# Performance work log

Hardware: AMD Instinct MI355X
Metric: run time of the kernel (lower is better)

Reference implementation:

```python
import jax, jax.numpy as jnp
import numpy as np

EPS = 1e-5

def setup_inputs() -> dict:
    key = jax.random.key(0)
    ks = jax.random.split(key, 7)
    C = 512
    x = jax.random.normal(ks[0], (16, C, 32, 32), dtype=jnp.float32)
    gn_w = jax.random.normal(ks[1], (C,), dtype=jnp.float32) * 0.02 + 1.0
    gn_b = jax.random.normal(ks[2], (C,), dtype=jnp.float32) * 0.02
    qkv_w = jax.random.normal(ks[3], (3 * C, C), dtype=jnp.float32) * (1.0 / np.sqrt(C))
    qkv_b = jax.random.normal(ks[4], (3 * C,), dtype=jnp.float32) * 0.02
    proj_w = jax.random.normal(ks[5], (C, C), dtype=jnp.float32) * (1.0 / np.sqrt(C))
    proj_b = jax.random.normal(ks[6], (C,), dtype=jnp.float32) * 0.02
    return {"x": x, "gn_w": gn_w, "gn_b": gn_b, "qkv_w": qkv_w,
            "qkv_b": qkv_b, "proj_w": proj_w, "proj_b": proj_b}

def reference(x, gn_w, gn_b, qkv_w, qkv_b, proj_w, proj_b):
    B, C, H, W = x.shape
    S = H * W
    # GroupNorm with 1 group: normalize over (C,H,W) per sample
    mean = jnp.mean(x, axis=(1, 2, 3), keepdims=True)
    var = jnp.var(x, axis=(1, 2, 3), keepdims=True)
    h = (x - mean) * jax.lax.rsqrt(var + EPS)
    h = h * gn_w[None, :, None, None] + gn_b[None, :, None, None]
    # 1x1 conv qkv: [B,C,H,W] -> [B,3C,H,W], flatten spatial -> [B,S,3C]
    hf = h.reshape(B, C, S)  # b c s
    qkv = jnp.einsum('bcs,oc->bso', hf, qkv_w) + qkv_b  # [B,S,3C]
    q, k, v = jnp.split(qkv, 3, axis=-1)  # each [B,S,C]
    scale = C ** (-0.5)
    attn = jax.nn.softmax(jnp.einsum('bqc,bkc->bqk', q, k) * scale, axis=-1)
    out = jnp.einsum('bqk,bkc->bqc', attn, v)  # [B,S,C]
    out = jnp.einsum('bsc,oc->bso', out, proj_w) + proj_b
    out = out.transpose(0, 2, 1).reshape(B, C, H, W)
    return x + out
```

## Files before the change

kernel.cpp:

```cpp
#include <hip/hip_runtime.h>
#include <stdint.h>

#define B_  16
#define C_  512
#define S_  1024
#define NSAMP (C_*S_)

typedef __bf16 bf16x8 __attribute__((ext_vector_type(8)));
typedef float  f32x4  __attribute__((ext_vector_type(4)));

__device__ __forceinline__ float bf2f(uint16_t u){ return __uint_as_float(((uint32_t)u)<<16); }
__device__ __forceinline__ uint16_t f2bf(float f){
  uint32_t u = __float_as_uint(f);
  uint32_t r = u + 0x7fffu + ((u>>16)&1u);
  return (uint16_t)(r>>16);
}
__device__ __forceinline__ float wsum(float v){
  #pragma unroll
  for(int o=32;o;o>>=1) v += __shfl_xor(v,o,64);
  return v;
}
__device__ __forceinline__ int wsumi(int v){
  #pragma unroll
  for(int o=32;o;o>>=1) v += __shfl_xor(v,o,64);
  return v;
}
__device__ __forceinline__ void gload16(const void* g, void* l){
  __builtin_amdgcn_global_load_lds(
      (__attribute__((address_space(1))) void*)g,
      (__attribute__((address_space(3))) void*)l, 16, 0, 0);
}

__device__ __forceinline__ void convseg(const void* src, uint16_t* dst, int n, int f, int t){
  const int idx = t*8;
  if (idx >= n) return;
  if (f){
    const float* s = (const float*)src;
    float4 v0 = *(const float4*)(s + idx);
    float4 v1 = *(const float4*)(s + idx + 4);
    ushort4 a, b;
    a.x=f2bf(v0.x); a.y=f2bf(v0.y); a.z=f2bf(v0.z); a.w=f2bf(v0.w);
    b.x=f2bf(v1.x); b.y=f2bf(v1.y); b.z=f2bf(v1.z); b.w=f2bf(v1.w);
    *(ushort4*)(dst + idx)     = a;
    *(ushort4*)(dst + idx + 4) = b;
  } else {
    *(uint4*)(dst + idx) = *(const uint4*)((const uint16_t*)src + idx);
  }
}
__global__ __launch_bounds__(256) void prep_k(
    const void* __restrict__ srcx, uint16_t* __restrict__ xb, float2* __restrict__ part,
    const void* qkvw, const void* projw, const void* gnw, const void* gnb,
    const void* qkvb, const void* projb,
    uint16_t* qkvwb, uint16_t* projwb, uint16_t* gnwb, uint16_t* gnbb,
    uint16_t* qkvbb, uint16_t* projbb, int* __restrict__ flag){
  const int t = threadIdx.x;
  __shared__ int sdet[4];
  int f;
  {
    const uint4 v = ((const uint4*)srcx)[t & 255];
    uint32_t ww[4] = {v.x, v.y, v.z, v.w};
    int c = 0;
    #pragma unroll
    for(int q=0;q<4;q++) c += ((((ww[q] & 0xffffu) >> 7) & 0xffu) >= 132) ? 1 : 0;
    c = wsumi(c);
    if ((t & 63) == 0) sdet[t >> 6] = c;
    __syncthreads();
    f = (sdet[0] + sdet[1] + sdet[2] + sdet[3] > 128) ? 1 : 0;
  }
  if (blockIdx.x == 0 && t == 0) *flag = f;

  if (blockIdx.x >= 1024){
    const int bid = blockIdx.x - 1024;
    if (bid < 384){
      const size_t off = (size_t)bid*2048;
      convseg((const char*)qkvw + off*(f?4:2), qkvwb + off, 2048, f, t);
    } else if (bid < 512){
      const size_t off = (size_t)(bid-384)*2048;
      convseg((const char*)projw + off*(f?4:2), projwb + off, 2048, f, t);
    } else {
      convseg(gnw,   gnwb,   512,  f, t);
      convseg(gnb,   gnbb,   512,  f, t);
      convseg(qkvb,  qkvbb,  1536, f, t);
      convseg(projb, projbb, 512,  f, t);
    }
    return;
  }
  const size_t base = (size_t)blockIdx.x * 8192;
  float s = 0.f, s2 = 0.f;
  if (f){
    const float4* sp = (const float4*)((const float*)srcx + base);
    ushort4* dp = (ushort4*)(xb + base);
    #pragma unroll
    for(int i=0;i<8;i++){
      float4 v = sp[i*256 + t];
      s  += v.x + v.y + v.z + v.w;
      s2 += v.x*v.x + v.y*v.y + v.z*v.z + v.w*v.w;
      ushort4 o; o.x=f2bf(v.x); o.y=f2bf(v.y); o.z=f2bf(v.z); o.w=f2bf(v.w);
      dp[i*256 + t] = o;
    }
  } else {
    const uint4* sp = (const uint4*)((const uint16_t*)srcx + base);
    uint4* dp = (uint4*)(xb + base);
    #pragma unroll
    for(int i=0;i<4;i++){
      uint4 p = sp[i*256 + t];
      dp[i*256 + t] = p;
      uint32_t uu[4] = {p.x,p.y,p.z,p.w};
      #pragma unroll
      for(int q=0;q<4;q++){
        float f0 = __uint_as_float(uu[q]<<16);
        float f1 = __uint_as_float(uu[q] & 0xffff0000u);
        s += f0 + f1; s2 += f0*f0 + f1*f1;
      }
    }
  }
  s = wsum(s); s2 = wsum(s2);
  __shared__ float rs[4], rq[4];
  const int lane = t & 63, w = t >> 6;
  if (lane==0){ rs[w]=s; rq[w]=s2; }
  __syncthreads();
  if (t==0)
    part[blockIdx.x] = make_float2(rs[0]+rs[1]+rs[2]+rs[3], rq[0]+rq[1]+rq[2]+rq[3]);
}

__global__ __launch_bounds__(256) void gn_apply_t(const uint16_t* __restrict__ x,
    const uint16_t* __restrict__ gw, const uint16_t* __restrict__ gb,
    const float2* __restrict__ part, uint16_t* __restrict__ hT){
  __shared__ float tile[64*129];
  const int b = blockIdx.z, c0 = blockIdx.y<<6, s0 = blockIdx.x<<7;
  const int t = threadIdx.x;
  float2 p = part[b*64 + (t & 63)];
  float s = wsum(p.x), s2 = wsum(p.y);
  const float ninv = 1.f/(float)NSAMP;
  const float mn = s*ninv;
  const float rstd = rsqrtf(s2*ninv - mn*mn + 1e-5f);
  #pragma unroll
  for(int k=0;k<4;k++){
    const int ci = t + k*256;
    const int cl = ci>>4, sc = ci&15;
    uint4 v = *(const uint4*)&x[((size_t)b*C_ + c0+cl)*S_ + s0 + sc*8];
    const uint16_t* e = (const uint16_t*)&v;
    float* dst = &tile[cl*129 + sc*8];
    #pragma unroll
    for(int q=0;q<8;q++) dst[q] = bf2f(e[q]);
  }
  __syncthreads();
  const int cc = t & 7;
  const int sb0 = t >> 3;
  uint4 wv4 = *(const uint4*)&gw[c0 + cc*8];
  uint4 bv4 = *(const uint4*)&gb[c0 + cc*8];
  const uint16_t* we = (const uint16_t*)&wv4;
  const uint16_t* be = (const uint16_t*)&bv4;
  float aq[8], cq[8];
  #pragma unroll
  for(int q=0;q<8;q++){ aq[q] = bf2f(we[q])*rstd; cq[q] = bf2f(be[q]) - mn*aq[q]; }
  #pragma unroll
  for(int k=0;k<4;k++){
    const int sl = sb0 + k*32;
    uint16_t ov[8];
    #pragma unroll
    for(int q=0;q<8;q++){
      float xv = tile[(cc*8+q)*129 + sl];
      ov[q] = f2bf(xv*aq[q] + cq[q]);
    }
    uint4 o;
    o.x = (uint32_t)ov[0] | ((uint32_t)ov[1]<<16);
    o.y = (uint32_t)ov[2] | ((uint32_t)ov[3]<<16);
    o.z = (uint32_t)ov[4] | ((uint32_t)ov[5]<<16);
    o.w = (uint32_t)ov[6] | ((uint32_t)ov[7]<<16);
    *(uint4*)&hT[((size_t)b*S_ + s0+sl)*C_ + c0 + cc*8] = o;
  }
}

__global__ __launch_bounds__(256)
void qkv_k(const uint16_t* __restrict__ hT, const uint16_t* __restrict__ qkvw,
           const uint16_t* __restrict__ qkvb, uint16_t* __restrict__ qk,
           uint16_t* __restrict__ Vt)
{
  __shared__ uint16_t smem[32768];
  const int tid = threadIdx.x;
  const int lane = tid & 63, w = tid >> 6;
  const int quad = lane >> 4, lm = lane & 15;
  const int wm = (w & 1) << 6, wn = (w >> 1) << 6;

  const bool vpath = blockIdx.x >= 1024;
  const int id = vpath ? (blockIdx.x - 1024) : blockIdx.x;
  const int r8 = id & 7, k8 = id >> 3;
  int m0, n0, bz;
  const uint16_t *Abase, *Bbase;
  if (!vpath){
    const int g = r8*16 + (k8 & 15);
    m0 = g << 7; n0 = (k8 >> 4) << 7; bz = 0;
    Abase = hT + (size_t)m0*512;
    Bbase = qkvw + (size_t)n0*512;
  } else {
    const int g = r8*16 + (k8 & 15);
    m0 = (k8 >> 4) << 7; n0 = (g & 7) << 7; bz = g >> 3;
    Abase = qkvw + (size_t)(1024 + m0)*512;
    Bbase = hT + (size_t)bz*S_*C_ + (size_t)n0*512;
  }

  f32x4 acc[4][4];
  #pragma unroll
  for(int i=0;i<4;i++)
    #pragma unroll
    for(int j=0;j<4;j++) acc[i][j] = (f32x4){0.f,0.f,0.f,0.f};

  const int srow = tid >> 3;
  const int sx   = (tid & 7) ^ (srow & 7);
  const uint16_t* ga = Abase + (size_t)srow*512 + sx*8;
  const uint16_t* gb = Bbase + (size_t)srow*512 + sx*8;
  uint16_t* sa0 = &smem[tid*8];
  uint16_t* sb0 = &smem[8192 + tid*8];
  uint16_t* sa1 = &smem[16384 + tid*8];
  uint16_t* sb1 = &smem[24576 + tid*8];

  #pragma unroll
  for(int i=0;i<4;i++){
    gload16(ga + (size_t)(i*32)*512, sa0 + i*2048);
    gload16(gb + (size_t)(i*32)*512, sb0 + i*2048);
  }
  for(int t=0;t<8;t++){
    if (t < 7){
      uint16_t* na = (t&1) ? sa0 : sa1;
      uint16_t* nb = (t&1) ? sb0 : sb1;
      const int k1 = (t+1)<<6;
      #pragma unroll
      for(int i=0;i<4;i++){
        gload16(ga + (size_t)(i*32)*512 + k1, na + i*2048);
        gload16(gb + (size_t)(i*32)*512 + k1, nb + i*2048);
      }
      asm volatile("s_waitcnt vmcnt(8)" ::: "memory");
    } else {
      asm volatile("s_waitcnt vmcnt(0)" ::: "memory");
    }
    __builtin_amdgcn_s_barrier();
    __builtin_amdgcn_sched_barrier(0);
    const int boff = (t&1) << 14;
    #pragma unroll
    for(int kk=0;kk<64;kk+=32){
      bf16x8 av[4], bv[4];
      #pragma unroll
      for(int i=0;i<4;i++){
        const int row = wm + i*16 + lm;
        av[i] = *(const bf16x8*)&smem[boff + row*64 + ((((kk>>3)+quad) ^ (row&7))<<3)];
      }
      #pragma unroll
      for(int j=0;j<4;j++){
        const int row = wn + j*16 + lm;
        bv[j] = *(const bf16x8*)&smem[boff + 8192 + row*64 + ((((kk>>3)+quad) ^ (row&7))<<3)];
      }
      #pragma unroll
      for(int i=0;i<4;i++)
        #pragma unroll
        for(int j=0;j<4;j++)
          acc[i][j] = __builtin_amdgcn_mfma_f32_16x16x32_bf16(av[i], bv[j], acc[i][j], 0,0,0);
    }
    __builtin_amdgcn_s_barrier();
  }

  uint16_t* Cs = smem;
  if (!vpath){
    #pragma unroll
    for(int j=0;j<4;j++){
      const int col_l = wn + j*16 + lm;
      const float bvv = bf2f(qkvb[n0 + col_l]);
      #pragma unroll
      for(int i=0;i<4;i++){
        const int rl0 = wm + i*16 + (quad<<2);
        #pragma unroll
        for(int r=0;r<4;r++)
          Cs[(rl0+r)*128 + col_l] = f2bf(acc[i][j][r] + bvv);
      }
    }
  } else {
    #pragma unroll
    for(int i=0;i<4;i++){
      const int rl0 = wm + i*16 + (quad<<2);
      #pragma unroll
      for(int r=0;r<4;r++){
        const float bvv = bf2f(qkvb[1024 + m0 + rl0 + r]);
        #pragma unroll
        for(int j=0;j<4;j++)
          Cs[(rl0+r)*128 + wn + j*16 + lm] = f2bf(acc[i][j][r] + bvv);
      }
    }
  }
  __syncthreads();
  uint16_t* base = vpath ? (Vt + (size_t)bz*C_*S_) : qk;
  #pragma unroll
  for(int k=0;k<8;k++){
    const int ci = tid + k*256;
    const int rl = ci>>4, ccc = ci&15;
    *(uint4*)&base[(size_t)(m0+rl)*1024 + n0 + ccc*8] = *(const uint4*)&Cs[rl*128 + ccc*8];
  }
}

__global__ __launch_bounds__(512)
void fa_k(const uint16_t* __restrict__ qk, const uint16_t* __restrict__ Vt,
          uint16_t* __restrict__ out)
{
  extern __shared__ char smem[];
  uint16_t* Qs = (uint16_t*)smem;
  char* Pb = smem + 65536;
  char* ST = smem + 81920;
  float* RS = (float*)(smem + 147456);

  const int tid = threadIdx.x;
  const int w = tid >> 6, lane = tid & 63;
  const int quad = lane >> 4, lm = lane & 15;
  const int wq = w & 1, wk = w >> 1;

  const int wg = (blockIdx.x & 7)*32 + (blockIdx.x >> 3);
  const int bz = wg >> 4;
  const int q0 = (wg & 15) << 6;

  const uint16_t* qbase = qk + ((size_t)bz*1024 + q0)*1024;
  const uint16_t* kbase = qk + (size_t)bz*1024*1024 + 512;
  const uint16_t* vbase = Vt + ((size_t)bz*512 + w*64)*1024;

  f32x4 o[4][4];
  #pragma unroll
  for(int i=0;i<4;i++)
    #pragma unroll
    for(int j=0;j<4;j++) o[i][j] = (f32x4){0.f,0.f,0.f,0.f};
  float rsacc[2][4];
  #pragma unroll
  for(int i=0;i<2;i++)
    #pragma unroll
    for(int r=0;r<4;r++) rsacc[i][r] = 0.f;

  auto stage_k = [&](int kt, int ch){
    #pragma unroll
    for (int g=0; g<2; ++g){
      const int idx = g*512 + tid;
      const int row = idx >> 3, c8 = idx & 7;
      gload16(kbase + (size_t)(kt*128 + row)*1024 + ch*64 + ((c8 ^ (row&7))<<3),
              ST + ((ch&3)<<14) + idx*16);
    }
  };
  auto stage_v = [&](int kt, int kk){
    #pragma unroll
    for (int g=0; g<4; ++g){
      const int idx = g*64 + lane;
      const int c = idx >> 2, c4 = idx & 3;
      gload16(vbase + (size_t)c*1024 + kt*128 + kk*32 + ((c4 ^ (c&3))<<3),
              ST + ((kk&1)<<15) + (w<<12) + idx*16);
    }
  };

  #pragma unroll
  for (int rd=0; rd<8; ++rd){
    const int row = rd*8 + (tid>>6), chunk = tid & 63;
    const int scol = (chunk & 56) | ((chunk & 7) ^ (row & 7));
    gload16(qbase + (size_t)row*1024 + scol*8, (char*)Qs + rd*8192 + tid*16);
  }
  stage_k(0,0); stage_k(0,1); stage_k(0,2);

  for (int kt=0; kt<8; ++kt){
    f32x4 s[2][2];
    #pragma unroll
    for(int i=0;i<2;i++)
      #pragma unroll
      for(int j=0;j<2;j++) s[i][j] = (f32x4){0.f,0.f,0.f,0.f};

    #pragma unroll
    for (int ch=0; ch<8; ++ch){
      if (ch==6) asm volatile("s_waitcnt vmcnt(2)" ::: "memory");
      else       asm volatile("s_waitcnt vmcnt(4)" ::: "memory");
      __builtin_amdgcn_s_barrier();
      __builtin_amdgcn_sched_barrier(0);
      if (ch < 5) stage_k(kt, ch+3);
      if (ch == 6) stage_v(kt, 0);
      const int slot = (ch&3)<<14;
      #pragma unroll
      for (int kk=0; kk<2; ++kk){
        bf16x8 av[2], bv[2];
        #pragma unroll
        for (int i=0;i<2;i++){
          const int q = wq*32 + i*16 + lm;
          av[i] = *(const bf16x8*)((const char*)Qs + q*1024 + (ch*8 + (((kk<<2)+quad) ^ (q&7)))*16);
        }
        #pragma unroll
        for (int j=0;j<2;j++){
          const int key = wk*32 + j*16 + lm;
          bv[j] = *(const bf16x8*)(ST + slot + key*128 + ((((kk<<2)+quad) ^ (key&7))<<4));
        }
        #pragma unroll
        for (int i=0;i<2;i++)
          #pragma unroll
          for (int j=0;j<2;j++)
            s[i][j] = __builtin_amdgcn_mfma_f32_16x16x32_bf16(av[i], bv[j], s[i][j], 0,0,0);
      }
    }

    #pragma unroll
    for (int i=0;i<2;i++)
      #pragma unroll
      for (int j=0;j<2;j++)
        #pragma unroll
        for (int r=0;r<4;r++){
          const int q = wq*32 + i*16 + (quad<<2) + r;
          const int col = wk*32 + j*16 + lm;
          const float pv = __expf(s[i][j][r] * 0.044194173824159216f);
          rsacc[i][r] += pv;
          const int cch = col >> 3;
          const int chs = (cch & 8) | ((cch & 7) ^ (q & 7));
          *(uint16_t*)(Pb + q*256 + chs*16 + ((col & 7)<<1)) = f2bf(pv);
        }
    asm volatile("s_waitcnt lgkmcnt(0)" ::: "memory");
    __builtin_amdgcn_sched_barrier(0);
    __builtin_amdgcn_s_barrier();
    __builtin_amdgcn_sched_barrier(0);
    stage_v(kt, 1);

    #pragma unroll
    for (int kk=0; kk<4; ++kk){
      if (kk<3) asm volatile("s_waitcnt vmcnt(4)" ::: "memory");
      else      asm volatile("s_waitcnt vmcnt(0)" ::: "memory");
      __builtin_amdgcn_sched_barrier(0);
      bf16x8 pa[4], bv[4];
      #pragma unroll
      for (int i=0;i<4;i++){
        const int q = i*16 + lm;
        const int cch = (kk<<2) + quad;
        const int chs = (cch & 8) | ((cch & 7) ^ (q & 7));
        pa[i] = *(const bf16x8*)(Pb + q*256 + chs*16);
      }
      #pragma unroll
      for (int j=0;j<4;j++){
        const int c = j*16 + lm;
        bv[j] = *(const bf16x8*)(ST + ((kk&1)<<15) + (w<<12) + c*64 + ((quad ^ (c&3))<<4));
      }
      #pragma unroll
      for (int i=0;i<4;i++)
        #pragma unroll
        for (int j=0;j<4;j++)
          o[i][j] = __builtin_amdgcn_mfma_f32_16x16x32_bf16(pa[i], bv[j], o[i][j], 0,0,0);
      __builtin_amdgcn_sched_barrier(0);
      if (kk<2) stage_v(kt, kk+2);
    }
    __builtin_amdgcn_s_barrier();
    if (kt < 7){ stage_k(kt+1,0); stage_k(kt+1,1); stage_k(kt+1,2); }
  }

  #pragma unroll
  for (int i=0;i<2;i++)
    #pragma unroll
    for (int r=0;r<4;r++){
      float v = rsacc[i][r];
      #pragma unroll
      for (int off=1; off<16; off<<=1) v += __shfl_xor(v, off, 64);
      rsacc[i][r] = v;
    }
  if (lm == 0){
    #pragma unroll
    for (int i=0;i<2;i++)
      #pragma unroll
      for (int r=0;r<4;r++){
        const int q = wq*32 + i*16 + (quad<<2) + r;
        RS[q*4 + wk] = rsacc[i][r];
      }
  }
  asm volatile("s_waitcnt lgkmcnt(0)" ::: "memory");
  __builtin_amdgcn_sched_barrier(0);
  __builtin_amdgcn_s_barrier();
  __builtin_amdgcn_sched_barrier(0);
  float inv_[4][4];
  #pragma unroll
  for (int i=0;i<4;i++)
    #pragma unroll
    for (int r=0;r<4;r++){
      const int q = i*16 + (quad<<2) + r;
      f32x4 rv = *(const f32x4*)&RS[q*4];
      inv_[i][r] = 1.f / (rv[0]+rv[1]+rv[2]+rv[3]);
    }
  uint16_t* Cs = Qs;
  #pragma unroll
  for (int i=0;i<4;i++)
    #pragma unroll
    for (int j=0;j<4;j++)
      #pragma unroll
      for (int r=0;r<4;r++){
        const int row = i*16 + (quad<<2) + r;
        const int col = (w<<6) + j*16 + lm;
        Cs[row*512 + col] = f2bf(o[i][j][r] * inv_[i][r]);
      }
  __syncthreads();
  #pragma unroll
  for (int rd=0; rd<8; ++rd){
    const int idx = rd*512 + tid;
    const int row = idx >> 6, cc = idx & 63;
    *(uint4*)&out[((size_t)bz*1024 + q0 + row)*512 + cc*8] =
        *(const uint4*)((const char*)Cs + row*1024 + cc*16);
  }
}

template<bool HASBIAS, bool BIASROW, bool OUTDYN, bool HASRES, int SWZMODE, bool EXP>
__global__ __launch_bounds__(256)
void gemm_bt(const uint16_t* __restrict__ A, const uint16_t* __restrict__ Bt,
             void* __restrict__ Cp, const uint16_t* __restrict__ bias,
             const uint16_t* __restrict__ xres, const int* __restrict__ flag,
             int lda, int ldb, int ldc, int K,
             long long sA, long long sB, long long sC)
{
  __shared__ uint16_t smem[32768];
  const int lin = (blockIdx.z * gridDim.y + blockIdx.y) * gridDim.x + blockIdx.x;
  const int r8 = lin & 7, kk8 = lin >> 3;
  int bx, by, bz;
  if (SWZMODE == 0){
    const int G = (gridDim.y * gridDim.z) >> 3;
    const int g = r8 * G + (kk8 % G);
    bx = kk8 / G; by = g % gridDim.y; bz = g / gridDim.y;
  } else {
    const int G = (gridDim.x * gridDim.z) >> 3;
    const int g = r8 * G + (kk8 % G);
    by = kk8 / G; bx = g % gridDim.x; bz = g / gridDim.x;
  }

  const int tid = threadIdx.x;
  const int lane = tid & 63, w = tid >> 6;
  const int quad = lane >> 4, lm = lane & 15;
  const int m0 = by << 7, n0 = bx << 7;
  A  += (size_t)bz * sA;
  Bt += (size_t)bz * sB;

  f32x4 acc[4][4];
  #pragma unroll
  for(int i=0;i<4;i++)
    #pragma unroll
    for(int j=0;j<4;j++) acc[i][j] = (f32x4){0.f,0.f,0.f,0.f};

  const int wm = (w & 1) << 6, wn = (w >> 1) << 6;
  const int srow = tid >> 3;
  const int sx   = (tid & 7) ^ (srow & 7);
  const uint16_t* ga = A  + (size_t)(m0 + srow)*lda + sx*8;
  const uint16_t* gb = Bt + (size_t)(n0 + srow)*ldb + sx*8;
  uint16_t* sa0 = &smem[tid*8];
  uint16_t* sb0 = &smem[8192 + tid*8];
  uint16_t* sa1 = &smem[16384 + tid*8];
  uint16_t* sb1 = &smem[24576 + tid*8];

  const int NT = K >> 6;
  #pragma unroll
  for(int i=0;i<4;i++){
    gload16(ga + (size_t)(i*32)*lda, sa0 + i*2048);
    gload16(gb + (size_t)(i*32)*ldb, sb0 + i*2048);
  }
  for(int t=0;t<NT;t++){
    if (t < NT-1){
      uint16_t* na = (t&1) ? sa0 : sa1;
      uint16_t* nb = (t&1) ? sb0 : sb1;
      const int k1 = (t+1)<<6;
      #pragma unroll
      for(int i=0;i<4;i++){
        gload16(ga + (size_t)(i*32)*lda + k1, na + i*2048);
        gload16(gb + (size_t)(i*32)*ldb + k1, nb + i*2048);
      }
      asm volatile("s_waitcnt vmcnt(8)" ::: "memory");
    } else {
      asm volatile("s_waitcnt vmcnt(0)" ::: "memory");
    }
    __builtin_amdgcn_s_barrier();
    __builtin_amdgcn_sched_barrier(0);
    const int boff = (t&1) << 14;
    #pragma unroll
    for(int kk=0;kk<64;kk+=32){
      bf16x8 av[4], bv[4];
      #pragma unroll
      for(int i=0;i<4;i++){
        const int row = wm + i*16 + lm;
        av[i] = *(const bf16x8*)&smem[boff + row*64 + ((((kk>>3)+quad) ^ (row&7))<<3)];
      }
      #pragma unroll
      for(int j=0;j<4;j++){
        const int row = wn + j*16 + lm;
        bv[j] = *(const bf16x8*)&smem[boff + 8192 + row*64 + ((((kk>>3)+quad) ^ (row&7))<<3)];
      }
      #pragma unroll
      for(int i=0;i<4;i++)
        #pragma unroll
        for(int j=0;j<4;j++)
          acc[i][j] = __builtin_amdgcn_mfma_f32_16x16x32_bf16(av[i], bv[j], acc[i][j], 0,0,0);
    }
    __builtin_amdgcn_s_barrier();
  }

  const size_t cb = (size_t)bz * (size_t)sC;
  if (!OUTDYN && !HASRES){
    uint16_t* Cs = smem;
    #pragma unroll
    for(int j=0;j<4;j++){
      const int col_l = wn + j*16 + lm;
      const float cbias = (HASBIAS && !BIASROW) ? bf2f(bias[n0 + col_l]) : 0.f;
      #pragma unroll
      for(int i=0;i<4;i++){
        const int rl0 = wm + i*16 + (quad<<2);
        #pragma unroll
        for(int r=0;r<4;r++){
          float v = acc[i][j][r] + cbias;
          if (HASBIAS && BIASROW) v += bf2f(bias[m0 + rl0 + r]);
          if (EXP) v = __expf(v * 0.044194173824159216f);
          Cs[(rl0+r)*128 + col_l] = f2bf(v);
        }
      }
    }
    __syncthreads();
    uint16_t* base = (uint16_t*)Cp + cb;
    #pragma unroll
    for(int k=0;k<8;k++){
      const int ci = tid + k*256;
      const int rl = ci>>4, cc = ci&15;
      *(uint4*)&base[(size_t)(m0+rl)*ldc + n0 + cc*8] = *(const uint4*)&Cs[rl*128 + cc*8];
    }
  } else {
    float* Cs32 = (float*)smem;
    const int f = OUTDYN ? *flag : 0;
    const int wnh = wn >> 1;
    #pragma unroll
    for(int half=0; half<2; ++half){
      #pragma unroll
      for(int j2=0;j2<2;j2++){
        const int j = half*2 + j2;
        const int col_l = wn + j*16 + lm;
        const int hcol = wnh + j2*16 + lm;
        const float cbias = (HASBIAS && !BIASROW) ? bf2f(bias[n0 + col_l]) : 0.f;
        #pragma unroll
        for(int i=0;i<4;i++){
          const int rl0 = wm + i*16 + (quad<<2);
          #pragma unroll
          for(int r=0;r<4;r++){
            float v = acc[i][j][r] + cbias;
            if (HASBIAS && BIASROW) v += bf2f(bias[m0 + rl0 + r]);
            if (EXP) v = __expf(v * 0.044194173824159216f);
            Cs32[(rl0+r)*64 + hcol] = v;
          }
        }
      }
      __syncthreads();
      #pragma unroll
      for(int k=0;k<8;k++){
        const int ci = tid + k*256;
        const int rl = ci>>4, c4 = ci&15;
        float4 vv = *(const float4*)&Cs32[rl*64 + c4*4];
        const int gcol = n0 + c4*4 + ((c4>=8)?32:0) + half*32;
        const size_t idx = cb + (size_t)(m0+rl)*ldc + gcol;
        float o0=vv.x, o1=vv.y, o2=vv.z, o3=vv.w;
        if (HASRES){
          uint2 rr = *(const uint2*)&xres[idx];
          o0 += bf2f((uint16_t)(rr.x & 0xffffu));
          o1 += bf2f((uint16_t)(rr.x >> 16));
          o2 += bf2f((uint16_t)(rr.y & 0xffffu));
          o3 += bf2f((uint16_t)(rr.y >> 16));
        }
        if (OUTDYN && f){
          float4 oo = make_float4(o0,o1,o2,o3);
          *(float4*)&((float*)Cp)[idx] = oo;
        } else {
          uint2 oo;
          oo.x = (uint32_t)f2bf(o0) | ((uint32_t)f2bf(o1)<<16);
          oo.y = (uint32_t)f2bf(o2) | ((uint32_t)f2bf(o3)<<16);
          *(uint2*)&((uint16_t*)Cp)[idx] = oo;
        }
      }
      __syncthreads();
    }
  }
}

extern "C" void kernel_launch(void* const* d_in, const int* in_sizes, int n_in,
                              void* d_out, int out_size, void* d_ws, size_t ws_size,
                              hipStream_t stream){
  char* ws = (char*)d_ws;
  int*      flag  = (int*)ws;
  float2*   part  = (float2*)(ws + 4096);
  uint16_t* gnwb  = (uint16_t*)(ws + 16384);
  uint16_t* gnbb  = (uint16_t*)(ws + 17408);
  uint16_t* qkvbb = (uint16_t*)(ws + 18432);
  uint16_t* projbb= (uint16_t*)(ws + 21504);
  uint16_t* qkvwb = (uint16_t*)(ws + 32768);
  uint16_t* projwb= (uint16_t*)(ws + 1605632);
  uint16_t* xb    = (uint16_t*)(ws + 4194304);
  uint16_t* hT    = (uint16_t*)(ws + 20971520);
  uint16_t* qk    = (uint16_t*)(ws + 37748736);
  uint16_t* Vt    = (uint16_t*)(ws + 104857600);

  static bool attr_done = false;
  if (!attr_done){
    (void)hipFuncSetAttribute(reinterpret_cast<const void*>(fa_k),
                              hipFuncAttributeMaxDynamicSharedMemorySize, 148480);
    attr_done = true;
  }

  hipLaunchKernelGGL(prep_k, dim3(1537), dim3(256), 0, stream,
                     d_in[0], xb, part,
                     d_in[3], d_in[5], d_in[1], d_in[2], d_in[4], d_in[6],
                     qkvwb, projwb, gnwb, gnbb, qkvbb, projbb, flag);
  hipLaunchKernelGGL(gn_apply_t, dim3(8,8,16), dim3(256), 0, stream, xb, gnwb, gnbb, part, hT);

  hipLaunchKernelGGL(qkv_k, dim3(1536), dim3(256), 0, stream, hT, qkvwb, qkvbb, qk, Vt);

  hipLaunchKernelGGL(fa_k, dim3(256), dim3(512), 148480, stream, qk, Vt, hT);

  hipLaunchKernelGGL((gemm_bt<true,true,true,true,1,false>), dim3(8,4,16), dim3(256), 0, stream,
      projwb, hT, d_out, projbb, xb, flag,
      512, 512, 1024, 512, 0LL, (long long)S_*C_, (long long)C_*S_);
}
```

Measured before the change: 205.2 us.

## Warp-specialize attention kernel into QK^T and PV wavefront groups

The attention kernel grows from 512 to 1024 threads and splits its wavefronts into two groups. Eight wavefronts compute QK^T and softmax numerators into a double-buffered P tile, while the other eight run the PV MFMAs one key tile behind, so the two phases overlap instead of being separated by block-wide barriers. Q is now read straight from global memory into registers rather than staged in LDS, and each wavefront stages its own K or V slices in private LDS buffers. The trade-offs are higher register pressure under launch_bounds(1024), a larger LDS footprint, and repeated global reads of Q.

```diff
diff --git a/kernel.cpp b/kernel.cpp
--- a/kernel.cpp
+++ b/kernel.cpp
@@ -296,28 +296,35 @@
   }
 }
 
-__global__ __launch_bounds__(512)
+__global__ __launch_bounds__(1024, 4)
 void fa_k(const uint16_t* __restrict__ qk, const uint16_t* __restrict__ Vt,
           uint16_t* __restrict__ out)
 {
   extern __shared__ char smem[];
-  uint16_t* Qs = (uint16_t*)smem;
-  char* Pb = smem + 65536;
-  char* ST = smem + 81920;
-  float* RS = (float*)(smem + 147456);
+  char* KST = smem;
+  char* VST = smem + 65536;
+  char* Pb  = smem + 131072;
+  float* RS = (float*)Pb;
 
   const int tid = threadIdx.x;
   const int w = tid >> 6, lane = tid & 63;
   const int quad = lane >> 4, lm = lane & 15;
-  const int wq = w & 1, wk = w >> 1;
 
   const int wg = (blockIdx.x & 7)*32 + (blockIdx.x >> 3);
   const int bz = wg >> 4;
   const int q0 = (wg & 15) << 6;
 
-  const uint16_t* qbase = qk + ((size_t)bz*1024 + q0)*1024;
+  const bool isQKT = (w < 8);
+  const int wq = w & 1, wk = (w >> 1) & 3;
+  const int pw = w & 7;
+
   const uint16_t* kbase = qk + (size_t)bz*1024*1024 + 512;
-  const uint16_t* vbase = Vt + ((size_t)bz*512 + w*64)*1024;
+  const uint16_t* qrow0 = qk + ((size_t)bz*1024 + q0 + wq*32 + lm)*1024 + quad*8;
+  const uint16_t* qrow1 = qrow0 + (size_t)16*1024;
+  const uint16_t* vbase = Vt + ((size_t)bz*512 + pw*64)*1024;
+
+  char* kpriv = KST + w*8192;
+  char* vpriv = VST + pw*8192;
 
   f32x4 o[4][4];
   #pragma unroll
@@ -330,166 +337,163 @@
     #pragma unroll
     for(int r=0;r<4;r++) rsacc[i][r] = 0.f;
 
-  auto stage_k = [&](int kt, int ch){
-    #pragma unroll
-    for (int g=0; g<2; ++g){
-      const int idx = g*512 + tid;
+  auto stage_kp = [&](int kt, int ch){
+    char* dst = kpriv + ((ch&1)<<12);
+    #pragma unroll
+    for (int g=0; g<4; ++g){
+      const int idx = g*64 + lane;
       const int row = idx >> 3, c8 = idx & 7;
-      gload16(kbase + (size_t)(kt*128 + row)*1024 + ch*64 + ((c8 ^ (row&7))<<3),
-              ST + ((ch&3)<<14) + idx*16);
+      gload16(kbase + (size_t)(kt*128 + wk*32 + row)*1024 + ch*64 + ((c8 ^ (row&7))<<3),
+              dst + idx*16);
     }
   };
-  auto stage_v = [&](int kt, int kk){
+  auto stage_vp = [&](int kt, int kk){
+    char* dst = vpriv + ((kk&1)<<12);
     #pragma unroll
     for (int g=0; g<4; ++g){
       const int idx = g*64 + lane;
       const int c = idx >> 2, c4 = idx & 3;
       gload16(vbase + (size_t)c*1024 + kt*128 + kk*32 + ((c4 ^ (c&3))<<3),
-              ST + ((kk&1)<<15) + (w<<12) + idx*16);
+              dst + idx*16);
     }
   };
 
-  #pragma unroll
-  for (int rd=0; rd<8; ++rd){
-    const int row = rd*8 + (tid>>6), chunk = tid & 63;
-    const int scol = (chunk & 56) | ((chunk & 7) ^ (row & 7));
-    gload16(qbase + (size_t)row*1024 + scol*8, (char*)Qs + rd*8192 + tid*16);
-  }
-  stage_k(0,0); stage_k(0,1); stage_k(0,2);
-
-  for (int kt=0; kt<8; ++kt){
-    f32x4 s[2][2];
-    #pragma unroll
-    for(int i=0;i<2;i++)
-      #pragma unroll
-      for(int j=0;j<2;j++) s[i][j] = (f32x4){0.f,0.f,0.f,0.f};
-
-    #pragma unroll
-    for (int ch=0; ch<8; ++ch){
-      if (ch==6) asm volatile("s_waitcnt vmcnt(2)" ::: "memory");
-      else       asm volatile("s_waitcnt vmcnt(4)" ::: "memory");
-      __builtin_amdgcn_s_barrier();
-      __builtin_amdgcn_sched_barrier(0);
-      if (ch < 5) stage_k(kt, ch+3);
-      if (ch == 6) stage_v(kt, 0);
-      const int slot = (ch&3)<<14;
-      #pragma unroll
-      for (int kk=0; kk<2; ++kk){
-        bf16x8 av[2], bv[2];
-        #pragma unroll
-        for (int i=0;i<2;i++){
-          const int q = wq*32 + i*16 + lm;
-          av[i] = *(const bf16x8*)((const char*)Qs + q*1024 + (ch*8 + (((kk<<2)+quad) ^ (q&7)))*16);
+  if (isQKT) stage_kp(0, 0);
+
+  for (int t=0; t<9; ++t){
+    __builtin_amdgcn_s_barrier();
+    if (isQKT){
+      if (t < 8){
+        f32x4 s[2][2];
+        #pragma unroll
+        for(int i=0;i<2;i++)
+          #pragma unroll
+          for(int j=0;j<2;j++) s[i][j] = (f32x4){0.f,0.f,0.f,0.f};
+        char* Pw = Pb + ((t&1)<<14);
+        #pragma unroll
+        for (int ch=0; ch<8; ++ch){
+          if (ch < 7)      stage_kp(t, ch+1);
+          else if (t < 7)  stage_kp(t+1, 0);
+          asm volatile("s_waitcnt vmcnt(4)" ::: "memory");
+          __builtin_amdgcn_sched_barrier(0);
+          const bf16x8 a00 = *(const bf16x8*)(qrow0 + ch*64);
+          const bf16x8 a10 = *(const bf16x8*)(qrow1 + ch*64);
+          const bf16x8 a01 = *(const bf16x8*)(qrow0 + ch*64 + 32);
+          const bf16x8 a11 = *(const bf16x8*)(qrow1 + ch*64 + 32);
+          const char* kslot = kpriv + ((ch&1)<<12);
+          #pragma unroll
+          for (int kk=0; kk<2; ++kk){
+            const int sw = (((kk<<2)+quad) ^ (lm&7)) << 4;
+            bf16x8 bv0 = *(const bf16x8*)(kslot + lm*128 + sw);
+            bf16x8 bv1 = *(const bf16x8*)(kslot + (16+lm)*128 + sw);
+            const bf16x8 A0 = kk ? a01 : a00;
+            const bf16x8 A1 = kk ? a11 : a10;
+            s[0][0] = __builtin_amdgcn_mfma_f32_16x16x32_bf16(A0, bv0, s[0][0], 0,0,0);
+            s[0][1] = __builtin_amdgcn_mfma_f32_16x16x32_bf16(A0, bv1, s[0][1], 0,0,0);
+            s[1][0] = __builtin_amdgcn_mfma_f32_16x16x32_bf16(A1, bv0, s[1][0], 0,0,0);
+            s[1][1] = __builtin_amdgcn_mfma_f32_16x16x32_bf16(A1, bv1, s[1][1], 0,0,0);
+          }
         }
         #pragma unroll
-        for (int j=0;j<2;j++){
-          const int key = wk*32 + j*16 + lm;
-          bv[j] = *(const bf16x8*)(ST + slot + key*128 + ((((kk<<2)+quad) ^ (key&7))<<4));
+        for (int i=0;i<2;i++)
+          #pragma unroll
+          for (int j=0;j<2;j++)
+            #pragma unroll
+            for (int r=0;r<4;r++){
+              const int q = wq*32 + i*16 + (quad<<2) + r;
+              const int col = wk*32 + j*16 + lm;
+              const float pv = __expf(s[i][j][r] * 0.044194173824159216f);
+              rsacc[i][r] += pv;
+              const int cch = col >> 3;
+              const int chs = (cch & 8) | ((cch & 7) ^ (q & 7));
+              *(uint16_t*)(Pw + q*256 + chs*16 + ((col & 7)<<1)) = f2bf(pv);
+            }
+        asm volatile("s_waitcnt lgkmcnt(0)" ::: "memory");
+      } else {
+        #pragma unroll
+        for (int i=0;i<2;i++)
+          #pragma unroll
+          for (int r=0;r<4;r++){
+            float v = rsacc[i][r];
+            #pragma unroll
+            for (int off=1; off<16; off<<=1) v += __shfl_xor(v, off, 64);
+            rsacc[i][r] = v;
+          }
+        if (lm == 0){
+          #pragma unroll
+          for (int i=0;i<2;i++)
+            #pragma unroll
+            for (int r=0;r<4;r++){
+              const int q = wq*32 + i*16 + (quad<<2) + r;
+              RS[q*4 + wk] = rsacc[i][r];
+            }
         }
-        #pragma unroll
-        for (int i=0;i<2;i++)
-          #pragma unroll
-          for (int j=0;j<2;j++)
-            s[i][j] = __builtin_amdgcn_mfma_f32_16x16x32_bf16(av[i], bv[j], s[i][j], 0,0,0);
-      }
-    }
-
-    #pragma unroll
-    for (int i=0;i<2;i++)
-      #pragma unroll
-      for (int j=0;j<2;j++)
+        asm volatile("s_waitcnt lgkmcnt(0)" ::: "memory");
+      }
+    } else {
+      if (t > 0){
+        const int kt = t-1;
+        const char* Pr = Pb + ((kt&1)<<14);
+        stage_vp(kt, 0);
+        stage_vp(kt, 1);
+        #pragma unroll
+        for (int kk=0; kk<4; ++kk){
+          if (kk < 3) asm volatile("s_waitcnt vmcnt(4)" ::: "memory");
+          else        asm volatile("s_waitcnt vmcnt(0)" ::: "memory");
+          __builtin_amdgcn_sched_barrier(0);
+          bf16x8 pa[4], bv[4];
+          #pragma unroll
+          for (int i=0;i<4;i++){
+            const int q = i*16 + lm;
+            const int cch = (kk<<2) + quad;
+            const int chs = (cch & 8) | ((cch & 7) ^ (q & 7));
+            pa[i] = *(const bf16x8*)(Pr + q*256 + chs*16);
+          }
+          #pragma unroll
+          for (int j=0;j<4;j++){
+            const int c = j*16 + lm;
+            bv[j] = *(const bf16x8*)(vpriv + ((kk&1)<<12) + c*64 + ((quad ^ (c&3))<<4));
+          }
+          #pragma unroll
+          for (int i=0;i<4;i++)
+            #pragma unroll
+            for (int j=0;j<4;j++)
+              o[i][j] = __builtin_amdgcn_mfma_f32_16x16x32_bf16(pa[i], bv[j], o[i][j], 0,0,0);
+          __builtin_amdgcn_sched_barrier(0);
+          if (kk < 2) stage_vp(kt, kk+2);
+        }
+      }
+    }
+  }
+
+  __builtin_amdgcn_s_barrier();
+  uint16_t* Cs = (uint16_t*)smem;
+  if (!isQKT){
+    float inv_[4][4];
+    #pragma unroll
+    for (int i=0;i<4;i++)
+      #pragma unroll
+      for (int r=0;r<4;r++){
+        const int q = i*16 + (quad<<2) + r;
+        f32x4 rv = *(const f32x4*)&RS[q*4];
+        inv_[i][r] = 1.f / (rv[0]+rv[1]+rv[2]+rv[3]);
+      }
+    #pragma unroll
+    for (int i=0;i<4;i++)
+      #pragma unroll
+      for (int j=0;j<4;j++)
         #pragma unroll
         for (int r=0;r<4;r++){
-          const int q = wq*32 + i*16 + (quad<<2) + r;
-          const int col = wk*32 + j*16 + lm;
-          const float pv = __expf(s[i][j][r] * 0.044194173824159216f);
-          rsacc[i][r] += pv;
-          const int cch = col >> 3;
-          const int chs = (cch & 8) | ((cch & 7) ^ (q & 7));
-          *(uint16_t*)(Pb + q*256 + chs*16 + ((col & 7)<<1)) = f2bf(pv);
+          const int row = i*16 + (quad<<2) + r;
+          const int col = pw*64 + j*16 + lm;
+          Cs[row*512 + col] = f2bf(o[i][j][r] * inv_[i][r]);
         }
-    asm volatile("s_waitcnt lgkmcnt(0)" ::: "memory");
-    __builtin_amdgcn_sched_barrier(0);
-    __builtin_amdgcn_s_barrier();
-    __builtin_amdgcn_sched_barrier(0);
-    stage_v(kt, 1);
-
-    #pragma unroll
-    for (int kk=0; kk<4; ++kk){
-      if (kk<3) asm volatile("s_waitcnt vmcnt(4)" ::: "memory");
-      else      asm volatile("s_waitcnt vmcnt(0)" ::: "memory");
-      __builtin_amdgcn_sched_barrier(0);
-      bf16x8 pa[4], bv[4];
-      #pragma unroll
-      for (int i=0;i<4;i++){
-        const int q = i*16 + lm;
-        const int cch = (kk<<2) + quad;
-        const int chs = (cch & 8) | ((cch & 7) ^ (q & 7));
-        pa[i] = *(const bf16x8*)(Pb + q*256 + chs*16);
-      }
-      #pragma unroll
-      for (int j=0;j<4;j++){
-        const int c = j*16 + lm;
-        bv[j] = *(const bf16x8*)(ST + ((kk&1)<<15) + (w<<12) + c*64 + ((quad ^ (c&3))<<4));
-      }
-      #pragma unroll
-      for (int i=0;i<4;i++)
-        #pragma unroll
-        for (int j=0;j<4;j++)
-          o[i][j] = __builtin_amdgcn_mfma_f32_16x16x32_bf16(pa[i], bv[j], o[i][j], 0,0,0);
-      __builtin_amdgcn_sched_barrier(0);
-      if (kk<2) stage_v(kt, kk+2);
-    }
-    __builtin_amdgcn_s_barrier();
-    if (kt < 7){ stage_k(kt+1,0); stage_k(kt+1,1); stage_k(kt+1,2); }
-  }
-
-  #pragma unroll
-  for (int i=0;i<2;i++)
-    #pragma unroll
-    for (int r=0;r<4;r++){
-      float v = rsacc[i][r];
-      #pragma unroll
-      for (int off=1; off<16; off<<=1) v += __shfl_xor(v, off, 64);
-      rsacc[i][r] = v;
-    }
-  if (lm == 0){
-    #pragma unroll
-    for (int i=0;i<2;i++)
-      #pragma unroll
-      for (int r=0;r<4;r++){
-        const int q = wq*32 + i*16 + (quad<<2) + r;
-        RS[q*4 + wk] = rsacc[i][r];
-      }
   }
   asm volatile("s_waitcnt lgkmcnt(0)" ::: "memory");
-  __builtin_amdgcn_sched_barrier(0);
   __builtin_amdgcn_s_barrier();
-  __builtin_amdgcn_sched_barrier(0);
-  float inv_[4][4];
-  #pragma unroll
-  for (int i=0;i<4;i++)
-    #pragma unroll
-    for (int r=0;r<4;r++){
-      const int q = i*16 + (quad<<2) + r;
-      f32x4 rv = *(const f32x4*)&RS[q*4];
-      inv_[i][r] = 1.f / (rv[0]+rv[1]+rv[2]+rv[3]);
-    }
-  uint16_t* Cs = Qs;
-  #pragma unroll
-  for (int i=0;i<4;i++)
-    #pragma unroll
-    for (int j=0;j<4;j++)
-      #pragma unroll
-      for (int r=0;r<4;r++){
-        const int row = i*16 + (quad<<2) + r;
-        const int col = (w<<6) + j*16 + lm;
-        Cs[row*512 + col] = f2bf(o[i][j][r] * inv_[i][r]);
-      }
-  __syncthreads();
-  #pragma unroll
-  for (int rd=0; rd<8; ++rd){
-    const int idx = rd*512 + tid;
+  #pragma unroll
+  for (int rd=0; rd<4; ++rd){
+    const int idx = rd*1024 + tid;
     const int row = idx >> 6, cc = idx & 63;
     *(uint4*)&out[((size_t)bz*1024 + q0 + row)*512 + cc*8] =
         *(const uint4*)((const char*)Cs + row*1024 + cc*16);
@@ -688,7 +692,7 @@
   static bool attr_done = false;
   if (!attr_done){
     (void)hipFuncSetAttribute(reinterpret_cast<const void*>(fa_k),
-                              hipFuncAttributeMaxDynamicSharedMemorySize, 148480);
+                              hipFuncAttributeMaxDynamicSharedMemorySize, 163840);
     attr_done = true;
   }
 
@@ -700,7 +704,7 @@
 
   hipLaunchKernelGGL(qkv_k, dim3(1536), dim3(256), 0, stream, hT, qkvwb, qkvbb, qk, Vt);
 
-  hipLaunchKernelGGL(fa_k, dim3(256), dim3(512), 148480, stream, qk, Vt, hT);
+  hipLaunchKernelGGL(fa_k, dim3(256), dim3(1024), 163840, stream, qk, Vt, hT);
 
   hipLaunchKernelGGL((gemm_bt<true,true,true,true,1,false>), dim3(8,4,16), dim3(256), 0, stream,
       projwb, hT, d_out, projbb, xb, flag,
```

After: 327.1 us. 59.4% more time.

## Hold Q in registers, read V directly from global, shrink LDS for occupancy

Applied to the files above, without the earlier changes.

The attention kernel now loads the Q tile into registers once instead of staging it in shared memory. V fragments are read straight from global memory instead of through an LDS staging pipeline, and the next tile's K prefetch moves into the tail of the current QK loop. Shared memory drops from about 145KB to 80KB and launch bounds ask for 2 blocks per CU, aiming at higher occupancy and less LDS traffic. The trade-off is heavy register pressure from the Q fragments, which may cause spills, plus uncoalesced global V loads that sit on the MFMA critical path with no explicit prefetch.

```diff
diff --git a/kernel.cpp b/kernel.cpp
--- a/kernel.cpp
+++ b/kernel.cpp
@@ -296,28 +296,39 @@
   }
 }
 
-__global__ __launch_bounds__(512)
+__global__ __launch_bounds__(512, 2)
 void fa_k(const uint16_t* __restrict__ qk, const uint16_t* __restrict__ Vt,
           uint16_t* __restrict__ out)
 {
   extern __shared__ char smem[];
-  uint16_t* Qs = (uint16_t*)smem;
+  char* ST = smem;
   char* Pb = smem + 65536;
-  char* ST = smem + 81920;
-  float* RS = (float*)(smem + 147456);
+  float* RS = (float*)Pb;
 
   const int tid = threadIdx.x;
   const int w = tid >> 6, lane = tid & 63;
   const int quad = lane >> 4, lm = lane & 15;
-  const int wq = w & 1, wk = w >> 1;
+  const int wq = w & 1, wk = (w >> 1) & 3;
 
   const int wg = (blockIdx.x & 7)*32 + (blockIdx.x >> 3);
   const int bz = wg >> 4;
   const int q0 = (wg & 15) << 6;
 
-  const uint16_t* qbase = qk + ((size_t)bz*1024 + q0)*1024;
   const uint16_t* kbase = qk + (size_t)bz*1024*1024 + 512;
   const uint16_t* vbase = Vt + ((size_t)bz*512 + w*64)*1024;
+
+  bf16x8 aq[2][8][2];
+  {
+    const uint16_t* qrow0 = qk + ((size_t)bz*1024 + q0 + wq*32 + lm)*1024 + quad*8;
+    const uint16_t* qrow1 = qrow0 + (size_t)16*1024;
+    #pragma unroll
+    for (int ch=0; ch<8; ++ch)
+      #pragma unroll
+      for (int kk=0; kk<2; ++kk){
+        aq[0][ch][kk] = *(const bf16x8*)(qrow0 + ch*64 + kk*32);
+        aq[1][ch][kk] = *(const bf16x8*)(qrow1 + ch*64 + kk*32);
+      }
+  }
 
   f32x4 o[4][4];
   #pragma unroll
@@ -339,22 +350,7 @@
               ST + ((ch&3)<<14) + idx*16);
     }
   };
-  auto stage_v = [&](int kt, int kk){
-    #pragma unroll
-    for (int g=0; g<4; ++g){
-      const int idx = g*64 + lane;
-      const int c = idx >> 2, c4 = idx & 3;
-      gload16(vbase + (size_t)c*1024 + kt*128 + kk*32 + ((c4 ^ (c&3))<<3),
-              ST + ((kk&1)<<15) + (w<<12) + idx*16);
-    }
-  };
-
-  #pragma unroll
-  for (int rd=0; rd<8; ++rd){
-    const int row = rd*8 + (tid>>6), chunk = tid & 63;
-    const int scol = (chunk & 56) | ((chunk & 7) ^ (row & 7));
-    gload16(qbase + (size_t)row*1024 + scol*8, (char*)Qs + rd*8192 + tid*16);
-  }
+
   stage_k(0,0); stage_k(0,1); stage_k(0,2);
 
   for (int kt=0; kt<8; ++kt){
@@ -366,31 +362,26 @@
 
     #pragma unroll
     for (int ch=0; ch<8; ++ch){
-      if (ch==6) asm volatile("s_waitcnt vmcnt(2)" ::: "memory");
-      else       asm volatile("s_waitcnt vmcnt(4)" ::: "memory");
+      if (ch < 6)       { asm volatile("s_waitcnt vmcnt(4)" ::: "memory"); }
+      else if (kt < 7)  { asm volatile("s_waitcnt vmcnt(4)" ::: "memory"); }
+      else if (ch == 6) { asm volatile("s_waitcnt vmcnt(2)" ::: "memory"); }
+      else              { asm volatile("s_waitcnt vmcnt(0)" ::: "memory"); }
       __builtin_amdgcn_s_barrier();
       __builtin_amdgcn_sched_barrier(0);
-      if (ch < 5) stage_k(kt, ch+3);
-      if (ch == 6) stage_v(kt, 0);
+      if (ch < 5)            stage_k(kt,   ch+3);
+      else if (kt < 7)       stage_k(kt+1, ch-5);
       const int slot = (ch&3)<<14;
       #pragma unroll
       for (int kk=0; kk<2; ++kk){
-        bf16x8 av[2], bv[2];
-        #pragma unroll
-        for (int i=0;i<2;i++){
-          const int q = wq*32 + i*16 + lm;
-          av[i] = *(const bf16x8*)((const char*)Qs + q*1024 + (ch*8 + (((kk<<2)+quad) ^ (q&7)))*16);
-        }
-        #pragma unroll
-        for (int j=0;j<2;j++){
-          const int key = wk*32 + j*16 + lm;
-          bv[j] = *(const bf16x8*)(ST + slot + key*128 + ((((kk<<2)+quad) ^ (key&7))<<4));
-        }
-        #pragma unroll
-        for (int i=0;i<2;i++)
-          #pragma unroll
-          for (int j=0;j<2;j++)
-            s[i][j] = __builtin_amdgcn_mfma_f32_16x16x32_bf16(av[i], bv[j], s[i][j], 0,0,0);
+        bf16x8 bv0, bv1;
+        const int key0 = wk*32 + lm;
+        const int key1 = key0 + 16;
+        bv0 = *(const bf16x8*)(ST + slot + key0*128 + ((((kk<<2)+quad) ^ (key0&7))<<4));
+        bv1 = *(const bf16x8*)(ST + slot + key1*128 + ((((kk<<2)+quad) ^ (key1&7))<<4));
+        s[0][0] = __builtin_amdgcn_mfma_f32_16x16x32_bf16(aq[0][ch][kk], bv0, s[0][0], 0,0,0);
+        s[0][1] = __builtin_amdgcn_mfma_f32_16x16x32_bf16(aq[0][ch][kk], bv1, s[0][1], 0,0,0);
+        s[1][0] = __builtin_amdgcn_mfma_f32_16x16x32_bf16(aq[1][ch][kk], bv0, s[1][0], 0,0,0);
+        s[1][1] = __builtin_amdgcn_mfma_f32_16x16x32_bf16(aq[1][ch][kk], bv1, s[1][1], 0,0,0);
       }
     }
 
@@ -412,13 +403,9 @@
     __builtin_amdgcn_sched_barrier(0);
     __builtin_amdgcn_s_barrier();
     __builtin_amdgcn_sched_barrier(0);
-    stage_v(kt, 1);
 
     #pragma unroll
     for (int kk=0; kk<4; ++kk){
-      if (kk<3) asm volatile("s_waitcnt vmcnt(4)" ::: "memory");
-      else      asm volatile("s_waitcnt vmcnt(0)" ::: "memory");
-      __builtin_amdgcn_sched_barrier(0);
       bf16x8 pa[4], bv[4];
       #pragma unroll
       for (int i=0;i<4;i++){
@@ -430,20 +417,17 @@
       #pragma unroll
       for (int j=0;j<4;j++){
         const int c = j*16 + lm;
-        bv[j] = *(const bf16x8*)(ST + ((kk&1)<<15) + (w<<12) + c*64 + ((quad ^ (c&3))<<4));
+        bv[j] = *(const bf16x8*)(vbase + (size_t)c*1024 + kt*128 + kk*32 + quad*8);
       }
       #pragma unroll
       for (int i=0;i<4;i++)
         #pragma unroll
         for (int j=0;j<4;j++)
           o[i][j] = __builtin_amdgcn_mfma_f32_16x16x32_bf16(pa[i], bv[j], o[i][j], 0,0,0);
-      __builtin_amdgcn_sched_barrier(0);
-      if (kk<2) stage_v(kt, kk+2);
-    }
-    __builtin_amdgcn_s_barrier();
-    if (kt < 7){ stage_k(kt+1,0); stage_k(kt+1,1); stage_k(kt+1,2); }
-  }
-
+    }
+  }
+
+  __builtin_amdgcn_s_barrier();
   #pragma unroll
   for (int i=0;i<2;i++)
     #pragma unroll
@@ -475,7 +459,8 @@
       f32x4 rv = *(const f32x4*)&RS[q*4];
       inv_[i][r] = 1.f / (rv[0]+rv[1]+rv[2]+rv[3]);
     }
-  uint16_t* Cs = Qs;
+  __builtin_amdgcn_s_barrier();
+  uint16_t* Cs = (uint16_t*)smem;
   #pragma unroll
   for (int i=0;i<4;i++)
     #pragma unroll
@@ -486,6 +471,7 @@
         const int col = (w<<6) + j*16 + lm;
         Cs[row*512 + col] = f2bf(o[i][j][r] * inv_[i][r]);
       }
+  asm volatile("s_waitcnt lgkmcnt(0)" ::: "memory");
   __syncthreads();
   #pragma unroll
   for (int rd=0; rd<8; ++rd){
@@ -688,7 +674,7 @@
   static bool attr_done = false;
   if (!attr_done){
     (void)hipFuncSetAttribute(reinterpret_cast<const void*>(fa_k),
-                              hipFuncAttributeMaxDynamicSharedMemorySize, 148480);
+                              hipFuncAttributeMaxDynamicSharedMemorySize, 81920);
     attr_done = true;
   }
 
@@ -700,7 +686,7 @@
 
   hipLaunchKernelGGL(qkv_k, dim3(1536), dim3(256), 0, stream, hT, qkvwb, qkvbb, qk, Vt);
 
-  hipLaunchKernelGGL(fa_k, dim3(256), dim3(512), 148480, stream, qk, Vt, hT);
+  hipLaunchKernelGGL(fa_k, dim3(256), dim3(512), 81920, stream, qk, Vt, hT);
 
   hipLaunchKernelGGL((gemm_bt<true,true,true,true,1,false>), dim3(8,4,16), dim3(256), 0, stream,
       projwb, hT, d_out, projbb, xb, flag,
```

Result: slower. 235.2 us (+14.6%).
